# Kernel tuning notes

Measured on AMD Instinct MI355X. Metric: run time of the kernel, lower is better.

The kernel has to match this reference:

```python
import jax, jax.numpy as jnp
import numpy as np

EPS = 1e-12  # F.normalize eps

def _l2norm(v, axis):
    n = jnp.sqrt(jnp.sum(v * v, axis=axis, keepdims=True))
    return v / jnp.maximum(n, EPS)

def setup_inputs() -> dict:
    key = jax.random.key(0)
    k1, k2, k3, k4 = jax.random.split(key, 4)
    B, N, D, K = 32, 8192, 128, 64
    x = jax.random.normal(k1, (B, N, D), dtype=jnp.float32)
    centroids = jnp.clip(0.01 * jax.random.normal(k2, (K, D), dtype=jnp.float32), -2.0, 2.0)
    conv_w = jax.random.normal(k3, (K, D), dtype=jnp.float32) / np.sqrt(D)
    conv_b = jax.random.normal(k4, (K,), dtype=jnp.float32) * 0.01
    return {"x": x, "centroids": centroids, "conv_w": conv_w, "conv_b": conv_b}

def reference(x, centroids, conv_w, conv_b):
    B, N, D = x.shape
    K = centroids.shape[0]
    # normalize_input: L2 over descriptor dim
    xn = _l2norm(x, axis=2)                                   # [B,N,D]
    # 1x1 conv == linear projection, softmax over clusters
    logits = jnp.einsum('bnd,kd->bnk', xn, conv_w) + conv_b   # [B,N,K]
    a = jax.nn.softmax(logits, axis=2)                        # [B,N,K]
    # vlad_{bkd} = sum_n a_{bnk} (x_{bnd} - c_{kd})
    #           = (a^T x)_{bkd} - c_{kd} * sum_n a_{bnk}
    ax = jnp.einsum('bnk,bnd->bkd', a, xn)                    # [B,K,D]
    a_sum = jnp.sum(a, axis=1)                                # [B,K]
    vlad = ax - centroids[None, :, :] * a_sum[:, :, None]     # [B,K,D]
    # intra-normalize, flatten, global normalize
    vlad = _l2norm(vlad, axis=2)
    vlad = vlad.reshape(B, K * D)
    vlad = _l2norm(vlad, axis=1)
    return vlad
```

## Files before the change

kernel.cpp:

```cpp
#include <hip/hip_runtime.h>
#include <math.h>

namespace {

typedef float f32x4 __attribute__((ext_vector_type(4)));
typedef float f32x16 __attribute__((ext_vector_type(16)));
typedef short bf16x8 __attribute__((ext_vector_type(8)));

constexpr int Bc = 32, Nc = 8192, Dc = 128, Kc = 64;
constexpr int PB = 16;
constexpr int RPB = Nc / PB;
constexpr int NT = 64;
constexpr int ITERS = RPB / NT;
constexpr int XSTR = 136;

__device__ __forceinline__ unsigned short f2bf(float f) {
  unsigned int u = __builtin_bit_cast(unsigned int, f);
  u = (u + 0x7FFFu + ((u >> 16) & 1u)) >> 16;
  return (unsigned short)u;
}
__device__ __forceinline__ unsigned int pk(float a, float b) {
  return (unsigned int)f2bf(a) | ((unsigned int)f2bf(b) << 16);
}

__global__ __launch_bounds__(256, 2) void nv_k1(
    const float* __restrict__ x, const float* __restrict__ conv_w,
    const float* __restrict__ conv_b, float* __restrict__ accP,
    float* __restrict__ asumP) {
  __shared__ __align__(16) short xS[NT * XSTR];
  __shared__ __align__(16) short aT[Kc * NT];
  __shared__ float asumS[4 * 64];

  const int tid = threadIdx.x;
  const int w = tid >> 6, l = tid & 63;
  const int bp = blockIdx.x;
  const int b = bp / PB, p = bp % PB;
  const float* xb = x + (size_t)b * Nc * Dc + (size_t)p * RPB * Dc;

  bf16x8 wf[4][4];
  float cb[4];
#pragma unroll
  for (int nt = 0; nt < 4; ++nt) {
    const int k = (l & 15) + 16 * nt;
    cb[nt] = conv_b[k];
#pragma unroll
    for (int ks = 0; ks < 4; ++ks) {
      const float* wp = conv_w + k * Dc + 8 * (l >> 4) + 32 * ks;
      const float4 w0 = *(const float4*)wp;
      const float4 w1 = *(const float4*)(wp + 4);
      union { unsigned int u[4]; bf16x8 v; } fu;
      fu.u[0] = pk(w0.x, w0.y); fu.u[1] = pk(w0.z, w0.w);
      fu.u[2] = pk(w1.x, w1.y); fu.u[3] = pk(w1.z, w1.w);
      wf[nt][ks] = fu.v;
    }
  }

  f32x16 acc2[2];
#pragma unroll
  for (int mt = 0; mt < 2; ++mt)
#pragma unroll
    for (int r = 0; r < 16; ++r) acc2[mt][r] = 0.f;
  float asum_acc[4] = {0.f, 0.f, 0.f, 0.f};

  const int sr = tid >> 2, sq = tid & 3;
  float4 cur[8];
  {
    const float* gp = xb + (size_t)sr * Dc + 32 * sq;
#pragma unroll
    for (int j = 0; j < 8; ++j) cur[j] = *(const float4*)(gp + 4 * j);
  }

  const int dcol = (l & 31) + 32 * w;

  for (int it = 0; it < ITERS; ++it) {
    float ss = 0.f;
#pragma unroll
    for (int j = 0; j < 8; ++j)
      ss += cur[j].x * cur[j].x + cur[j].y * cur[j].y +
            cur[j].z * cur[j].z + cur[j].w * cur[j].w;
    ss += __shfl_xor(ss, 1);
    ss += __shfl_xor(ss, 2);
    const float invn = 1.0f / fmaxf(sqrtf(ss), 1e-12f);
    unsigned int xv[16];
#pragma unroll
    for (int j = 0; j < 8; ++j) {
      xv[2 * j] = pk(cur[j].x * invn, cur[j].y * invn);
      xv[2 * j + 1] = pk(cur[j].z * invn, cur[j].w * invn);
    }
    __syncthreads();
    {
      short* dst = xS + sr * XSTR + 32 * sq;
#pragma unroll
      for (int j = 0; j < 4; ++j) {
        union { unsigned int u[4]; bf16x8 v; } fu;
        fu.u[0] = xv[4 * j]; fu.u[1] = xv[4 * j + 1];
        fu.u[2] = xv[4 * j + 2]; fu.u[3] = xv[4 * j + 3];
        *(bf16x8*)(dst + 8 * j) = fu.v;
      }
    }
    if (it + 1 < ITERS) {
      const float* gp = xb + (size_t)((it + 1) * NT + sr) * Dc + 32 * sq;
#pragma unroll
      for (int j = 0; j < 8; ++j) cur[j] = *(const float4*)(gp + 4 * j);
    }
    __syncthreads();

    f32x4 c1[4];
#pragma unroll
    for (int nt = 0; nt < 4; ++nt) {
      c1[nt][0] = 0.f; c1[nt][1] = 0.f; c1[nt][2] = 0.f; c1[nt][3] = 0.f;
    }
#pragma unroll
    for (int ks = 0; ks < 4; ++ks) {
      const bf16x8 af =
          *(const bf16x8*)(xS + (16 * w + (l & 15)) * XSTR + 8 * (l >> 4) + 32 * ks);
#pragma unroll
      for (int nt = 0; nt < 4; ++nt)
        c1[nt] = __builtin_amdgcn_mfma_f32_16x16x32_bf16(af, wf[nt][ks],
                                                         c1[nt], 0, 0, 0);
    }

    float a4[4][4];
#pragma unroll
    for (int nt = 0; nt < 4; ++nt)
#pragma unroll
      for (int i = 0; i < 4; ++i) a4[nt][i] = c1[nt][i] + cb[nt];
#pragma unroll
    for (int i = 0; i < 4; ++i) {
      float mx = fmaxf(fmaxf(a4[0][i], a4[1][i]), fmaxf(a4[2][i], a4[3][i]));
      mx = fmaxf(mx, __shfl_xor(mx, 1));
      mx = fmaxf(mx, __shfl_xor(mx, 2));
      mx = fmaxf(mx, __shfl_xor(mx, 4));
      mx = fmaxf(mx, __shfl_xor(mx, 8));
      float s = 0.f;
#pragma unroll
      for (int nt = 0; nt < 4; ++nt) {
        a4[nt][i] = __expf(a4[nt][i] - mx);
        s += a4[nt][i];
      }
      s += __shfl_xor(s, 1);
      s += __shfl_xor(s, 2);
      s += __shfl_xor(s, 4);
      s += __shfl_xor(s, 8);
      const float inv = __builtin_amdgcn_rcpf(s);
#pragma unroll
      for (int nt = 0; nt < 4; ++nt) a4[nt][i] *= inv;
    }
#pragma unroll
    for (int nt = 0; nt < 4; ++nt) {
      float s = a4[nt][0] + a4[nt][1] + a4[nt][2] + a4[nt][3];
      s += __shfl_xor(s, 16);
      s += __shfl_xor(s, 32);
      asum_acc[nt] += s;
      const int k = (l & 15) + 16 * nt;
      const int cn = 4 * w + (l >> 4);
      const unsigned int u0 = pk(a4[nt][0], a4[nt][1]);
      const unsigned int u1 = pk(a4[nt][2], a4[nt][3]);
      *(uint2*)(aT + k * NT + ((cn ^ (l & 15)) << 2)) = make_uint2(u0, u1);
    }
    __syncthreads();

#pragma unroll
    for (int ks2 = 0; ks2 < 4; ++ks2) {
      const int n0 = 16 * ks2 + 8 * (l >> 5);
      union { unsigned int u[4]; bf16x8 v; } bu;
#pragma unroll
      for (int j = 0; j < 4; ++j) {
        const unsigned short s0 =
            *(const unsigned short*)(xS + (n0 + 2 * j) * XSTR + dcol);
        const unsigned short s1 =
            *(const unsigned short*)(xS + (n0 + 2 * j + 1) * XSTR + dcol);
        bu.u[j] = (unsigned int)s0 | ((unsigned int)s1 << 16);
      }
#pragma unroll
      for (int mt = 0; mt < 2; ++mt) {
        const int k = (l & 31) + 32 * mt;
        const int cn = n0 >> 2;
        const uint2 lo = *(const uint2*)(aT + k * NT + (((cn)     ^ (k & 15)) << 2));
        const uint2 hi = *(const uint2*)(aT + k * NT + (((cn + 1) ^ (k & 15)) << 2));
        union { unsigned int u[4]; bf16x8 v; } au;
        au.u[0] = lo.x; au.u[1] = lo.y; au.u[2] = hi.x; au.u[3] = hi.y;
        acc2[mt] = __builtin_amdgcn_mfma_f32_32x32x16_bf16(au.v, bu.v,
                                                           acc2[mt], 0, 0, 0);
      }
    }
  }

#pragma unroll
  for (int nt = 0; nt < 4; ++nt)
    if (l < 16) asumS[w * 64 + nt * 16 + (l & 15)] = asum_acc[nt];
  __syncthreads();
  if (tid < 64)
    asumP[(size_t)bp * Kc + tid] =
        asumS[tid] + asumS[64 + tid] + asumS[128 + tid] + asumS[192 + tid];

  float* ap = accP + (size_t)bp * (Kc * Dc);
#pragma unroll
  for (int mt = 0; mt < 2; ++mt)
#pragma unroll
    for (int r = 0; r < 16; ++r) {
      const int k = 32 * mt + (r & 3) + 8 * (r >> 2) + 4 * (l >> 5);
      ap[k * Dc + dcol] = acc2[mt][r];
    }
}

__global__ __launch_bounds__(256) void nv_k2(
    const float* __restrict__ accP, const float* __restrict__ asumP,
    const float* __restrict__ cent, float* __restrict__ out,
    float* __restrict__ gssP) {
  __shared__ float asumS[8];
  __shared__ float redS[8][17];
  __shared__ float gssWv[4];
  const int tid = threadIdx.x;
  const int w = tid >> 6, l = tid & 63;
  const int b = blockIdx.x >> 3;
  const int kg = blockIdx.x & 7;

  if (tid < 128)
    redS[tid >> 4][tid & 15] =
        asumP[(size_t)(b * PB + (tid & 15)) * Kc + kg * 8 + (tid >> 4)];
  __syncthreads();
  if (tid < 8) {
    float s = 0.f;
#pragma unroll
    for (int q = 0; q < 16; ++q) s += redS[tid][q];
    asumS[tid] = s;
  }
  __syncthreads();

  float gss = 0.f;
#pragma unroll
  for (int ki = 0; ki < 2; ++ki) {
    const int kloc = w + 4 * ki, k = kg * 8 + kloc;
    float v0 = 0.f, v1 = 0.f;
    for (int pp = 0; pp < PB; ++pp) {
      const float2 t = *(const float2*)(accP + (size_t)(b * PB + pp) * (Kc * Dc) +
                                        k * Dc + 2 * l);
      v0 += t.x;
      v1 += t.y;
    }
    const float as = asumS[kloc];
    const float2 c2 = *(const float2*)(cent + (size_t)k * Dc + 2 * l);
    v0 -= c2.x * as;
    v1 -= c2.y * as;
    float ssk = v0 * v0 + v1 * v1;
#pragma unroll
    for (int o = 1; o < 64; o <<= 1) ssk += __shfl_xor(ssk, o);
    const float sc = 1.0f / fmaxf(sqrtf(ssk), 1e-12f);
    gss += ssk * sc * sc;
    float2* o2 =
        reinterpret_cast<float2*>(out + (size_t)b * (Kc * Dc) + k * Dc + 2 * l);
    *o2 = make_float2(v0 * sc, v1 * sc);
  }
  if (l == 0) gssWv[w] = gss;
  __syncthreads();
  if (tid == 0) gssP[blockIdx.x] = gssWv[0] + gssWv[1] + gssWv[2] + gssWv[3];
}

__global__ __launch_bounds__(256) void nv_k3(float* __restrict__ out,
                                             const float* __restrict__ gssP) {
  const int bid = blockIdx.x;
  const int b = bid >> 3;
  float g = 0.f;
#pragma unroll
  for (int i = 0; i < 8; ++i) g += gssP[b * 8 + i];
  const float gsc = 1.0f / fmaxf(sqrtf(g), 1e-12f);
  float4* o4 = reinterpret_cast<float4*>(out) + (size_t)bid * 256 + threadIdx.x;
  float4 v = *o4;
  v.x *= gsc;
  v.y *= gsc;
  v.z *= gsc;
  v.w *= gsc;
  *o4 = v;
}

}

extern "C" void kernel_launch(void* const* d_in, const int* in_sizes, int n_in,
                              void* d_out, int out_size, void* d_ws,
                              size_t ws_size, hipStream_t stream) {
  const float* x = (const float*)d_in[0];
  const float* ce = (const float*)d_in[1];
  const float* cw = (const float*)d_in[2];
  const float* cb = (const float*)d_in[3];
  float* out = (float*)d_out;

  const size_t accPf = (size_t)Bc * PB * Kc * Dc;
  const size_t asumPf = (size_t)Bc * PB * Kc;
  float* accP = (float*)d_ws;
  float* asumP = accP + accPf;
  float* gssP = asumP + asumPf;

  nv_k1<<<Bc * PB, 256, 0, stream>>>(x, cw, cb, accP, asumP);
  nv_k2<<<Bc * 8, 256, 0, stream>>>(accP, asumP, ce, out, gssP);
  nv_k3<<<256, 256, 0, stream>>>(out, gssP);
}
```

Measured before the change: 53.65 us.

## Reduce split-N partials with global atomics and double the row splits

Instead of writing per-block partial [K,D] accumulators to workspace and summing them in the second kernel, each block now atomically adds its partial into a single per-batch accumulator, which is zeroed with a memset beforehand. The N-split factor is doubled and the occupancy hint raised so more blocks run at once. The bf16 conversion now uses the HIP intrinsic. This removes the large partial-buffer write and re-read but adds atomic contention, an extra memset launch, and order-dependent float summation.

```diff
diff --git a/kernel.cpp b/kernel.cpp
--- a/kernel.cpp
+++ b/kernel.cpp
@@ -1,4 +1,5 @@
 #include <hip/hip_runtime.h>
+#include <hip/hip_bf16.h>
 #include <math.h>
 
 namespace {
@@ -8,25 +9,22 @@
 typedef short bf16x8 __attribute__((ext_vector_type(8)));
 
 constexpr int Bc = 32, Nc = 8192, Dc = 128, Kc = 64;
-constexpr int PB = 16;
+constexpr int PB = 32;
 constexpr int RPB = Nc / PB;
 constexpr int NT = 64;
 constexpr int ITERS = RPB / NT;
 constexpr int XSTR = 136;
 
-__device__ __forceinline__ unsigned short f2bf(float f) {
-  unsigned int u = __builtin_bit_cast(unsigned int, f);
-  u = (u + 0x7FFFu + ((u >> 16) & 1u)) >> 16;
-  return (unsigned short)u;
-}
 __device__ __forceinline__ unsigned int pk(float a, float b) {
-  return (unsigned int)f2bf(a) | ((unsigned int)f2bf(b) << 16);
-}
-
-__global__ __launch_bounds__(256, 2) void nv_k1(
+  union { __hip_bfloat162 h; unsigned int u; } c;
+  c.h = __float22bfloat162_rn(make_float2(a, b));
+  return c.u;
+}
+
+__global__ __launch_bounds__(256, 4) void nv_k1(
     const float* __restrict__ x, const float* __restrict__ conv_w,
-    const float* __restrict__ conv_b, float* __restrict__ accP,
-    float* __restrict__ asumP) {
+    const float* __restrict__ conv_b, float* __restrict__ accA,
+    float* __restrict__ asumA) {
   __shared__ __align__(16) short xS[NT * XSTR];
   __shared__ __align__(16) short aT[Kc * NT];
   __shared__ float asumS[4 * 64];
@@ -191,58 +189,42 @@
     if (l < 16) asumS[w * 64 + nt * 16 + (l & 15)] = asum_acc[nt];
   __syncthreads();
   if (tid < 64)
-    asumP[(size_t)bp * Kc + tid] =
-        asumS[tid] + asumS[64 + tid] + asumS[128 + tid] + asumS[192 + tid];
-
-  float* ap = accP + (size_t)bp * (Kc * Dc);
+    atomicAdd(&asumA[(size_t)b * Kc + tid],
+              asumS[tid] + asumS[64 + tid] + asumS[128 + tid] + asumS[192 + tid]);
+
+  float* ap = accA + (size_t)b * (Kc * Dc);
 #pragma unroll
   for (int mt = 0; mt < 2; ++mt)
 #pragma unroll
     for (int r = 0; r < 16; ++r) {
       const int k = 32 * mt + (r & 3) + 8 * (r >> 2) + 4 * (l >> 5);
-      ap[k * Dc + dcol] = acc2[mt][r];
+      atomicAdd(&ap[k * Dc + dcol], acc2[mt][r]);
     }
 }
 
 __global__ __launch_bounds__(256) void nv_k2(
-    const float* __restrict__ accP, const float* __restrict__ asumP,
+    const float* __restrict__ accA, const float* __restrict__ asumA,
     const float* __restrict__ cent, float* __restrict__ out,
     float* __restrict__ gssP) {
   __shared__ float asumS[8];
-  __shared__ float redS[8][17];
   __shared__ float gssWv[4];
   const int tid = threadIdx.x;
   const int w = tid >> 6, l = tid & 63;
   const int b = blockIdx.x >> 3;
   const int kg = blockIdx.x & 7;
 
-  if (tid < 128)
-    redS[tid >> 4][tid & 15] =
-        asumP[(size_t)(b * PB + (tid & 15)) * Kc + kg * 8 + (tid >> 4)];
-  __syncthreads();
-  if (tid < 8) {
-    float s = 0.f;
-#pragma unroll
-    for (int q = 0; q < 16; ++q) s += redS[tid][q];
-    asumS[tid] = s;
-  }
+  if (tid < 8) asumS[tid] = asumA[(size_t)b * Kc + kg * 8 + tid];
   __syncthreads();
 
   float gss = 0.f;
 #pragma unroll
   for (int ki = 0; ki < 2; ++ki) {
     const int kloc = w + 4 * ki, k = kg * 8 + kloc;
-    float v0 = 0.f, v1 = 0.f;
-    for (int pp = 0; pp < PB; ++pp) {
-      const float2 t = *(const float2*)(accP + (size_t)(b * PB + pp) * (Kc * Dc) +
-                                        k * Dc + 2 * l);
-      v0 += t.x;
-      v1 += t.y;
-    }
+    const float2 t = *(const float2*)(accA + (size_t)b * (Kc * Dc) + k * Dc + 2 * l);
     const float as = asumS[kloc];
     const float2 c2 = *(const float2*)(cent + (size_t)k * Dc + 2 * l);
-    v0 -= c2.x * as;
-    v1 -= c2.y * as;
+    float v0 = t.x - c2.x * as;
+    float v1 = t.y - c2.y * as;
     float ssk = v0 * v0 + v1 * v1;
 #pragma unroll
     for (int o = 1; o < 64; o <<= 1) ssk += __shfl_xor(ssk, o);
@@ -285,13 +267,14 @@
   const float* cb = (const float*)d_in[3];
   float* out = (float*)d_out;
 
-  const size_t accPf = (size_t)Bc * PB * Kc * Dc;
-  const size_t asumPf = (size_t)Bc * PB * Kc;
-  float* accP = (float*)d_ws;
-  float* asumP = accP + accPf;
-  float* gssP = asumP + asumPf;
-
-  nv_k1<<<Bc * PB, 256, 0, stream>>>(x, cw, cb, accP, asumP);
-  nv_k2<<<Bc * 8, 256, 0, stream>>>(accP, asumP, ce, out, gssP);
+  const size_t accf = (size_t)Bc * Kc * Dc;
+  const size_t asumf = (size_t)Bc * Kc;
+  float* accA = (float*)d_ws;
+  float* asumA = accA + accf;
+  float* gssP = asumA + asumf;
+
+  (void)hipMemsetAsync(d_ws, 0, (accf + asumf) * sizeof(float), stream);
+  nv_k1<<<Bc * PB, 256, 0, stream>>>(x, cw, cb, accA, asumA);
+  nv_k2<<<Bc * 8, 256, 0, stream>>>(accA, asumA, ce, out, gssP);
   nv_k3<<<256, 256, 0, stream>>>(out, gssP);
 }
```

New measurement: 110.7 us. 106% more time.
